# Kernel optimization log

Measured on AMD Instinct MI355X. Metric: run time of the kernel, lower is better.

## Reference

```python
import jax, jax.numpy as jnp
import numpy as np

EMBED_DIM = 1024
BATCH = 4
SEQ = 2048


def setup_inputs() -> dict:
    key = jax.random.key(0)
    ks = jax.random.split(key, 9)
    D = EMBED_DIM
    s = 1.0 / np.sqrt(D)
    inputs = jax.random.normal(ks[0], (BATCH, SEQ, D), dtype=jnp.float32)
    rotation_params = jax.random.normal(ks[1], (D, D), dtype=jnp.float32) * s
    entangle_params = jax.random.normal(ks[2], (D, D), dtype=jnp.float32) * s
    Wq = jax.random.normal(ks[3], (D, D), dtype=jnp.float32) * s
    bq = jax.random.normal(ks[4], (D,), dtype=jnp.float32) * 0.01
    Wk = jax.random.normal(ks[5], (D, D), dtype=jnp.float32) * s
    bk = jax.random.normal(ks[6], (D,), dtype=jnp.float32) * 0.01
    Wv = jax.random.normal(ks[7], (D, D), dtype=jnp.float32) * s
    bv = jax.random.normal(ks[8], (D,), dtype=jnp.float32) * 0.01
    # causal mask: True = masked out (matches torch masked_fill semantics)
    mask = jnp.triu(jnp.ones((SEQ, SEQ), dtype=bool), k=1)
    return {"inputs": inputs, "rotation_params": rotation_params,
            "entangle_params": entangle_params, "Wq": Wq, "bq": bq,
            "Wk": Wk, "bk": bk, "Wv": Wv, "bv": bv, "mask": mask}


def reference(inputs, rotation_params, entangle_params, Wq, bq, Wk, bk, Wv, bv, mask):
    D = inputs.shape[-1]
    # q = Linear(x) @ R^T ; k = Linear(x) @ E^T ; v = Linear(x)
    q = (jnp.einsum('bsd,ed->bse', inputs, Wq) + bq) @ rotation_params.T
    k = (jnp.einsum('bsd,ed->bse', inputs, Wk) + bk) @ entangle_params.T
    v = jnp.einsum('bsd,ed->bse', inputs, Wv) + bv
    scores = jnp.einsum('bqd,bkd->bqk', q, k) / jnp.sqrt(jnp.float32(D))
    scores = jnp.where(mask, jnp.float32(-jnp.inf), scores)
    probs = jax.nn.softmax(scores, axis=-1)  # dropout=0.0 -> identity
    return jnp.einsum('bqk,bkd->bqd', probs, v)
```

## Files before the change

kernel.cpp:

```cpp
#include <hip/hip_runtime.h>
#include <hip/hip_bf16.h>
#include <stdint.h>

#define DD 1024
#define SS 2048
#define BB 4

typedef __bf16 bf16;
typedef __bf16 bf16x8 __attribute__((ext_vector_type(8)));
typedef __bf16 bf16x4 __attribute__((ext_vector_type(4)));
typedef float f32x4 __attribute__((ext_vector_type(4)));

__device__ __forceinline__ void gload_lds16(const bf16* g, bf16* l) {
  __builtin_amdgcn_global_load_lds(
      (const __attribute__((address_space(1))) void*)g,
      (__attribute__((address_space(3))) void*)l, 16, 0, 0);
}

__global__ void cvt_all(const float* __restrict__ x, const float* __restrict__ R,
                        const float* __restrict__ E, const float* __restrict__ Wv,
                        bf16* __restrict__ xb, bf16* __restrict__ Rb,
                        bf16* __restrict__ Eb, bf16* __restrict__ Wvb) {
  int bid = blockIdx.x;
  const float* src;
  bf16* dst;
  int base;
  if (bid < 8192) { src = x; dst = xb; base = bid; }
  else if (bid < 9216) { src = R; dst = Rb; base = bid - 8192; }
  else if (bid < 10240) { src = E; dst = Eb; base = bid - 9216; }
  else { src = Wv; dst = Wvb; base = bid - 10240; }
  int i = (base * 256 + threadIdx.x) * 4;
  float4 v = *(const float4*)(src + i);
  bf16x4 o;
  o.x = (bf16)v.x; o.y = (bf16)v.y; o.z = (bf16)v.z; o.w = (bf16)v.w;
  *(bf16x4*)(dst + i) = o;
}

__global__ void transpose_cvt(const float* __restrict__ Wq,
                              const float* __restrict__ Wk,
                              bf16* __restrict__ WqT, bf16* __restrict__ WkT) {
  const float* src = blockIdx.z ? Wk : Wq;
  bf16* dst = blockIdx.z ? WkT : WqT;
  __shared__ float tile[32][33];
  int x = blockIdx.x * 32 + threadIdx.x;
  int y0 = blockIdx.y * 32;
  for (int r = threadIdx.y; r < 32; r += 8)
    tile[r][threadIdx.x] = src[(y0 + r) * DD + x];
  __syncthreads();
  int dx = blockIdx.y * 32 + threadIdx.x;
  int dy0 = blockIdx.x * 32;
  for (int r = threadIdx.y; r < 32; r += 8)
    dst[(dy0 + r) * DD + dx] = (bf16)tile[threadIdx.x][r];
}

__global__ void bias_fold(const float* __restrict__ R, const float* __restrict__ bq,
                          const float* __restrict__ E, const float* __restrict__ bk,
                          const float* __restrict__ bv, float* __restrict__ bias) {
  int e = blockIdx.x;
  if (e >= 2048) { if (threadIdx.x == 0) bias[e] = bv[e - 2048]; return; }
  const float* M = (e < 1024) ? R : E;
  const float* bb = (e < 1024) ? bq : bk;
  int row = e & 1023;
  float s = 0.f;
  for (int f = threadIdx.x; f < DD; f += 256) s += M[row * DD + f] * bb[f];
  for (int o = 32; o >= 1; o >>= 1) s += __shfl_xor(s, o, 64);
  __shared__ float red[4];
  if ((threadIdx.x & 63) == 0) red[threadIdx.x >> 6] = s;
  __syncthreads();
  if (threadIdx.x == 0) bias[e] = red[0] + red[1] + red[2] + red[3];
}

template <int MODE>
__global__ __launch_bounds__(256, 4)
void gemm_bt(const bf16* __restrict__ Ag, long lda, long sAb,
             const bf16* __restrict__ Bg, long ldb, long sBb,
             void* __restrict__ Cg, long ldc, long sCb,
             const float* __restrict__ bias, float scale, int K,
             bf16* __restrict__ vTp) {
  __shared__ __align__(16) bf16 smem[16384];
  bf16* As = smem;
  bf16* Bs = smem + 8192;

  int bx = blockIdx.x, by = blockIdx.y, bz = blockIdx.z;
  if (MODE == 1 && bx > by) return;
  long m0 = (long)by * 128, n0 = (long)bx * 128;
  const bf16* A = Ag + (long)bz * sAb + m0 * lda;
  const bf16* Bp = Bg + (long)bz * sBb + n0 * ldb;

  int t = threadIdx.x;
  int w = t >> 6, l = t & 63;
  int lr = l >> 2;
  int lc = (((l & 3) ^ (lr & 3)) * 8);
  int quad = l >> 4, ln = l & 15;
  int wm = w >> 1, wn = w & 1;
  int rdoff = ((quad ^ (ln & 3)) * 8);

  int Keff = (MODE == 2) ? (by + 1) * 128 : K;

  f32x4 acc[4][4];
#pragma unroll
  for (int i = 0; i < 4; i++)
#pragma unroll
    for (int j = 0; j < 4; j++) acc[i][j] = f32x4{0.f, 0.f, 0.f, 0.f};

  const bf16* a_base = As + (wm * 64 + ln) * 32 + rdoff;
  const bf16* b_base = Bs + (wn * 64 + ln) * 32 + rdoff;
  long arow0 = (long)(w * 16 + lr);

  for (int k0 = 0; k0 < Keff; k0 += 64) {
#pragma unroll
    for (int kk = 0; kk < 2; kk++) {
      int kc = k0 + kk * 32 + lc;
      gload_lds16(A + arow0 * lda + kc, As + kk * 4096 + w * 512);
      gload_lds16(A + (arow0 + 64) * lda + kc, As + kk * 4096 + 2048 + w * 512);
      gload_lds16(Bp + arow0 * ldb + kc, Bs + kk * 4096 + w * 512);
      gload_lds16(Bp + (arow0 + 64) * ldb + kc, Bs + kk * 4096 + 2048 + w * 512);
    }
    asm volatile("s_waitcnt vmcnt(0)" ::: "memory");
    __syncthreads();

#pragma unroll
    for (int kk = 0; kk < 2; kk++) {
      bf16x8 af[4], bfr[4];
#pragma unroll
      for (int i = 0; i < 4; i++) {
        af[i] = *(const bf16x8*)(a_base + kk * 4096 + i * 512);
        bfr[i] = *(const bf16x8*)(b_base + kk * 4096 + i * 512);
      }
#pragma unroll
      for (int i = 0; i < 4; i++)
#pragma unroll
        for (int j = 0; j < 4; j++)
          acc[i][j] = __builtin_amdgcn_mfma_f32_16x16x32_bf16(
              af[i], bfr[j], acc[i][j], 0, 0, 0);
    }
    __syncthreads();
  }

  if (MODE == 0) {
    if (vTp && n0 >= 2048) {
      int d0 = (int)n0 - 2048;
      int b = (int)(m0 >> 11);
      int s0 = (int)(m0 & 2047);
#pragma unroll
      for (int i = 0; i < 4; i++) {
        int sb = wm * 64 + i * 16 + quad * 4;
#pragma unroll
        for (int j = 0; j < 4; j++) {
          int d = wn * 64 + j * 16 + ln;
          float bv_ = bias[n0 + d];
#pragma unroll
          for (int r = 0; r < 4; r++)
            smem[d * 128 + ((sb + r) ^ (ln << 3))] = (bf16)(acc[i][j][r] + bv_);
        }
      }
      __syncthreads();
      int d = t >> 1, h = t & 1;
      bf16* dst = vTp + (long)b * DD * SS + (long)(d0 + d) * SS + s0 + h * 64;
#pragma unroll
      for (int j = 0; j < 8; j++) {
        int sbase = h * 64 + j * 8;
        bf16x8 v = *(const bf16x8*)(smem + d * 128 + (sbase ^ ((d & 15) << 3)));
        *(bf16x8*)(dst + j * 8) = v;
      }
    } else {
      bf16* C = (bf16*)Cg + (long)bz * sCb + m0 * ldc + n0;
#pragma unroll
      for (int i = 0; i < 4; i++) {
        int rb = wm * 64 + i * 16 + quad * 4;
#pragma unroll
        for (int j = 0; j < 4; j++) {
          int col = wn * 64 + j * 16 + ln;
          float bv_ = bias ? bias[n0 + col] : 0.f;
#pragma unroll
          for (int r = 0; r < 4; r++)
            C[(long)(rb + r) * ldc + col] = (bf16)(acc[i][j][r] + bv_);
        }
      }
    }
  } else {
    float* C = (float*)Cg + (long)bz * sCb + m0 * ldc + n0;
#pragma unroll
    for (int i = 0; i < 4; i++) {
      int rb = wm * 64 + i * 16 + quad * 4;
#pragma unroll
      for (int j = 0; j < 4; j++) {
        int col = wn * 64 + j * 16 + ln;
#pragma unroll
        for (int r = 0; r < 4; r++) {
          int row = rb + r;
          if (MODE == 1) {
            if (n0 + col <= m0 + row)
              C[(long)row * ldc + col] = acc[i][j][r] * scale;
          } else {
            C[(long)row * ldc + col] = acc[i][j][r];
          }
        }
      }
    }
  }
}

__global__ __launch_bounds__(256) void softmax_rows(float* __restrict__ scores) {
  long m = blockIdx.x;
  int i = (int)(m & (SS - 1));
  float* row = scores + m * SS;
  int t = threadIdx.x;
  int nvalid = i + 1;
  int base = t * 8;
  float x[8] = {0, 0, 0, 0, 0, 0, 0, 0};
  if (base < nvalid) {
    float4 v0 = *(const float4*)(row + base);
    float4 v1 = *(const float4*)(row + base + 4);
    x[0] = v0.x; x[1] = v0.y; x[2] = v0.z; x[3] = v0.w;
    x[4] = v1.x; x[5] = v1.y; x[6] = v1.z; x[7] = v1.w;
  }

  float mx = -INFINITY;
#pragma unroll
  for (int j = 0; j < 8; j++)
    if (base + j < nvalid) mx = fmaxf(mx, x[j]);
  for (int o = 32; o >= 1; o >>= 1) mx = fmaxf(mx, __shfl_xor(mx, o, 64));
  __shared__ float red[8];
  if ((t & 63) == 0) red[t >> 6] = mx;
  __syncthreads();
  mx = fmaxf(fmaxf(red[0], red[1]), fmaxf(red[2], red[3]));

  float e[8];
  float sum = 0.f;
#pragma unroll
  for (int j = 0; j < 8; j++) {
    e[j] = (base + j < nvalid) ? __expf(x[j] - mx) : 0.f;
    sum += e[j];
  }
  for (int o = 32; o >= 1; o >>= 1) sum += __shfl_xor(sum, o, 64);
  if ((t & 63) == 0) red[4 + (t >> 6)] = sum;
  __syncthreads();
  sum = red[4] + red[5] + red[6] + red[7];
  float inv = 1.f / sum;

  bf16x8 o8;
#pragma unroll
  for (int j = 0; j < 8; j++) o8[j] = (bf16)(e[j] * inv);
  *(bf16x8*)((bf16*)row + base) = o8;
}

extern "C" void kernel_launch(void* const* d_in, const int* in_sizes, int n_in,
                              void* d_out, int out_size, void* d_ws,
                              size_t ws_size, hipStream_t stream) {
  const float* x = (const float*)d_in[0];
  const float* R = (const float*)d_in[1];
  const float* E = (const float*)d_in[2];
  const float* Wq = (const float*)d_in[3];
  const float* bq = (const float*)d_in[4];
  const float* Wk = (const float*)d_in[5];
  const float* bk = (const float*)d_in[6];
  const float* Wv = (const float*)d_in[7];
  const float* bv = (const float*)d_in[8];
  float* out = (float*)d_out;

  char* ws = (char*)d_ws;
  bf16* qkv = (bf16*)ws;
  bf16* vT = (bf16*)(ws + 50331648);
  float* scores = (float*)(ws + 67108864);
  char* sr = ws + 67108864;
  bf16* xb = (bf16*)sr;
  bf16* Rb = (bf16*)(sr + 16777216);
  bf16* WqT = (bf16*)(sr + 20971520);
  bf16* wcat = (bf16*)(sr + 25165824);
  float* bias = (float*)(sr + 31457280);
  bf16* Eb = Rb + 1024 * 1024;
  bf16* WkT = WqT + 1024 * 1024;

  cvt_all<<<11264, 256, 0, stream>>>(x, R, E, Wv, xb, Rb, Eb, wcat + 2048 * DD);
  transpose_cvt<<<dim3(32, 32, 2), dim3(32, 8), 0, stream>>>(Wq, Wk, WqT, WkT);
  bias_fold<<<3072, 256, 0, stream>>>(R, bq, E, bk, bv, bias);

  gemm_bt<0><<<dim3(8, 8, 2), 256, 0, stream>>>(
      Rb, DD, 1024 * 1024, WqT, DD, 1024 * 1024, wcat, DD, 1024 * 1024,
      nullptr, 1.f, DD, nullptr);

  gemm_bt<0><<<dim3(24, 64, 1), 256, 0, stream>>>(xb, DD, 0, wcat, DD, 0, qkv,
                                                  3072, 0, bias, 1.f, DD, vT);

  gemm_bt<1><<<dim3(16, 16, BB), 256, 0, stream>>>(
      qkv, 3072, (long)SS * 3072, qkv + 1024, 3072, (long)SS * 3072, scores,
      SS, (long)SS * SS, nullptr, 0.03125f, DD, nullptr);

  softmax_rows<<<BB * SS, 256, 0, stream>>>(scores);

  gemm_bt<2><<<dim3(8, 16, BB), 256, 0, stream>>>(
      (const bf16*)scores, 4096, (long)SS * 4096, vT, SS, (long)DD * SS, out,
      DD, (long)SS * DD, nullptr, 1.f, SS, nullptr);
}
```

Measured before the change: 311.5 us.

## Add 256x128-tile GEMM with 32x32 MFMA for QKV and score products

Adds a new gemm_big kernel that uses 256x128 output tiles, a 64-wide K step, and 32x32x16 bf16 MFMA instructions. The QKV projection (including the transposed V write) and the causal QK^T score GEMM now use it. The larger tiles are meant to raise operand reuse and arithmetic intensity per LDS load, and the new MFMA shape issues fewer instructions. In exchange, occupancy drops (launch bounds 2), the grids have fewer blocks, and the causal skip works at coarser granularity, so more fully masked work may be computed.

```diff
diff --git a/kernel.cpp b/kernel.cpp
--- a/kernel.cpp
+++ b/kernel.cpp
@@ -10,6 +10,7 @@
 typedef __bf16 bf16x8 __attribute__((ext_vector_type(8)));
 typedef __bf16 bf16x4 __attribute__((ext_vector_type(4)));
 typedef float f32x4 __attribute__((ext_vector_type(4)));
+typedef float f32x16 __attribute__((ext_vector_type(16)));
 
 __device__ __forceinline__ void gload_lds16(const bf16* g, bf16* l) {
   __builtin_amdgcn_global_load_lds(
@@ -71,18 +72,145 @@
 }
 
 template <int MODE>
+__global__ __launch_bounds__(256, 2)
+void gemm_big(const bf16* __restrict__ Ag, long lda, long sAb,
+              const bf16* __restrict__ Bg, long ldb, long sBb,
+              void* __restrict__ Cg, long ldc, long sCb,
+              const float* __restrict__ bias, float scale, int K,
+              bf16* __restrict__ vTp) {
+  __shared__ __align__(16) bf16 As[256 * 64];
+  __shared__ __align__(16) bf16 Bs[128 * 64];
+
+  int bx = blockIdx.x, by = blockIdx.y, bz = blockIdx.z;
+  if (MODE == 1 && bx > 2 * by + 1) return;
+  long m0 = (long)by * 256, n0 = (long)bx * 128;
+  const bf16* A = Ag + (long)bz * sAb + m0 * lda;
+  const bf16* Bp = Bg + (long)bz * sBb + n0 * ldb;
+
+  int t = threadIdx.x;
+  int w = t >> 6, l = t & 63;
+  int lrow = l >> 3, lch = l & 7;
+  int swz = (lch ^ lrow) * 8;
+  int rl = l & 31, kh = l >> 5;
+  int wm = w >> 1, wn = w & 1;
+
+  f32x16 acc[4][2];
+#pragma unroll
+  for (int g = 0; g < 4; g++)
+#pragma unroll
+    for (int h = 0; h < 2; h++)
+#pragma unroll
+      for (int rr = 0; rr < 16; rr++) acc[g][h][rr] = 0.f;
+
+  for (int k0 = 0; k0 < K; k0 += 64) {
+#pragma unroll
+    for (int i = 0; i < 8; i++) {
+      int r0 = w * 64 + i * 8;
+      gload_lds16(A + (long)(r0 + lrow) * lda + k0 + swz, As + r0 * 64);
+    }
+#pragma unroll
+    for (int i = 0; i < 4; i++) {
+      int r0 = w * 32 + i * 8;
+      gload_lds16(Bp + (long)(r0 + lrow) * ldb + k0 + swz, Bs + r0 * 64);
+    }
+    asm volatile("s_waitcnt vmcnt(0)" ::: "memory");
+    __syncthreads();
+
+#pragma unroll
+    for (int kk = 0; kk < 4; kk++) {
+      int pos = ((kk * 2 + kh) ^ (rl & 7)) * 8;
+      bf16x8 af[4], bfr[2];
+#pragma unroll
+      for (int g = 0; g < 4; g++)
+        af[g] = *(const bf16x8*)(As + (wm * 128 + g * 32 + rl) * 64 + pos);
+#pragma unroll
+      for (int h = 0; h < 2; h++)
+        bfr[h] = *(const bf16x8*)(Bs + (wn * 64 + h * 32 + rl) * 64 + pos);
+#pragma unroll
+      for (int g = 0; g < 4; g++)
+#pragma unroll
+        for (int h = 0; h < 2; h++)
+          acc[g][h] = __builtin_amdgcn_mfma_f32_32x32x16_bf16(
+              af[g], bfr[h], acc[g][h], 0, 0, 0);
+    }
+    __syncthreads();
+  }
+
+  if (MODE == 0) {
+    if (vTp && n0 >= 2048) {
+      int d0 = (int)n0 - 2048;
+      int b = (int)(m0 >> 11);
+      int s0 = (int)(m0 & 2047);
+#pragma unroll
+      for (int hs = 0; hs < 2; hs++) {
+        if (wm == hs) {
+#pragma unroll
+          for (int g = 0; g < 4; g++)
+#pragma unroll
+            for (int h = 0; h < 2; h++) {
+              int d = wn * 64 + h * 32 + rl;
+              float bv_ = bias[n0 + d];
+#pragma unroll
+              for (int rr = 0; rr < 16; rr++) {
+                int s = g * 32 + (rr & 3) + 8 * (rr >> 2) + 4 * kh;
+                As[d * 128 + (s ^ ((d & 15) << 3))] = (bf16)(acc[g][h][rr] + bv_);
+              }
+            }
+        }
+        __syncthreads();
+        int d = t >> 1, hc = t & 1;
+        bf16* dst = vTp + (long)b * DD * SS + (long)(d0 + d) * SS + s0 + hs * 128;
+#pragma unroll
+        for (int j = 0; j < 8; j++) {
+          int sb = hc * 64 + j * 8;
+          bf16x8 v = *(const bf16x8*)(As + d * 128 + (sb ^ ((d & 15) << 3)));
+          *(bf16x8*)(dst + sb) = v;
+        }
+        __syncthreads();
+      }
+    } else {
+      bf16* C = (bf16*)Cg + (long)bz * sCb + m0 * ldc + n0;
+#pragma unroll
+      for (int g = 0; g < 4; g++)
+#pragma unroll
+        for (int h = 0; h < 2; h++) {
+          int col = wn * 64 + h * 32 + rl;
+          float bv_ = bias ? bias[n0 + col] : 0.f;
+#pragma unroll
+          for (int rr = 0; rr < 16; rr++) {
+            int row = wm * 128 + g * 32 + (rr & 3) + 8 * (rr >> 2) + 4 * kh;
+            C[(long)row * ldc + col] = (bf16)(acc[g][h][rr] + bv_);
+          }
+        }
+    }
+  } else {
+    float* C = (float*)Cg + (long)bz * sCb + m0 * ldc + n0;
+#pragma unroll
+    for (int g = 0; g < 4; g++)
+#pragma unroll
+      for (int h = 0; h < 2; h++) {
+        int col = wn * 64 + h * 32 + rl;
+#pragma unroll
+        for (int rr = 0; rr < 16; rr++) {
+          int row = wm * 128 + g * 32 + (rr & 3) + 8 * (rr >> 2) + 4 * kh;
+          if (n0 + col <= m0 + row)
+            C[(long)row * ldc + col] = acc[g][h][rr] * scale;
+        }
+      }
+  }
+}
+
+template <int MODE>
 __global__ __launch_bounds__(256, 4)
 void gemm_bt(const bf16* __restrict__ Ag, long lda, long sAb,
              const bf16* __restrict__ Bg, long ldb, long sBb,
              void* __restrict__ Cg, long ldc, long sCb,
-             const float* __restrict__ bias, float scale, int K,
-             bf16* __restrict__ vTp) {
+             const float* __restrict__ bias, float scale, int K) {
   __shared__ __align__(16) bf16 smem[16384];
   bf16* As = smem;
   bf16* Bs = smem + 8192;
 
   int bx = blockIdx.x, by = blockIdx.y, bz = blockIdx.z;
-  if (MODE == 1 && bx > by) return;
   long m0 = (long)by * 128, n0 = (long)bx * 128;
   const bf16* A = Ag + (long)bz * sAb + m0 * lda;
   const bf16* Bp = Bg + (long)bz * sBb + n0 * ldb;
@@ -138,44 +266,17 @@
   }
 
   if (MODE == 0) {
-    if (vTp && n0 >= 2048) {
-      int d0 = (int)n0 - 2048;
-      int b = (int)(m0 >> 11);
-      int s0 = (int)(m0 & 2047);
-#pragma unroll
-      for (int i = 0; i < 4; i++) {
-        int sb = wm * 64 + i * 16 + quad * 4;
-#pragma unroll
-        for (int j = 0; j < 4; j++) {
-          int d = wn * 64 + j * 16 + ln;
-          float bv_ = bias[n0 + d];
-#pragma unroll
-          for (int r = 0; r < 4; r++)
-            smem[d * 128 + ((sb + r) ^ (ln << 3))] = (bf16)(acc[i][j][r] + bv_);
-        }
-      }
-      __syncthreads();
-      int d = t >> 1, h = t & 1;
-      bf16* dst = vTp + (long)b * DD * SS + (long)(d0 + d) * SS + s0 + h * 64;
-#pragma unroll
-      for (int j = 0; j < 8; j++) {
-        int sbase = h * 64 + j * 8;
-        bf16x8 v = *(const bf16x8*)(smem + d * 128 + (sbase ^ ((d & 15) << 3)));
-        *(bf16x8*)(dst + j * 8) = v;
-      }
-    } else {
-      bf16* C = (bf16*)Cg + (long)bz * sCb + m0 * ldc + n0;
-#pragma unroll
-      for (int i = 0; i < 4; i++) {
-        int rb = wm * 64 + i * 16 + quad * 4;
-#pragma unroll
-        for (int j = 0; j < 4; j++) {
-          int col = wn * 64 + j * 16 + ln;
-          float bv_ = bias ? bias[n0 + col] : 0.f;
-#pragma unroll
-          for (int r = 0; r < 4; r++)
-            C[(long)(rb + r) * ldc + col] = (bf16)(acc[i][j][r] + bv_);
-        }
+    bf16* C = (bf16*)Cg + (long)bz * sCb + m0 * ldc + n0;
+#pragma unroll
+    for (int i = 0; i < 4; i++) {
+      int rb = wm * 64 + i * 16 + quad * 4;
+#pragma unroll
+      for (int j = 0; j < 4; j++) {
+        int col = wn * 64 + j * 16 + ln;
+        float bv_ = bias ? bias[n0 + col] : 0.f;
+#pragma unroll
+        for (int r = 0; r < 4; r++)
+          C[(long)(rb + r) * ldc + col] = (bf16)(acc[i][j][r] + bv_);
       }
     }
   } else {
@@ -187,15 +288,8 @@
       for (int j = 0; j < 4; j++) {
         int col = wn * 64 + j * 16 + ln;
 #pragma unroll
-        for (int r = 0; r < 4; r++) {
-          int row = rb + r;
-          if (MODE == 1) {
-            if (n0 + col <= m0 + row)
-              C[(long)row * ldc + col] = acc[i][j][r] * scale;
-          } else {
-            C[(long)row * ldc + col] = acc[i][j][r];
-          }
-        }
+        for (int r = 0; r < 4; r++)
+          C[(long)(rb + r) * ldc + col] = acc[i][j][r];
       }
     }
   }
@@ -278,12 +372,12 @@
 
   gemm_bt<0><<<dim3(8, 8, 2), 256, 0, stream>>>(
       Rb, DD, 1024 * 1024, WqT, DD, 1024 * 1024, wcat, DD, 1024 * 1024,
-      nullptr, 1.f, DD, nullptr);
-
-  gemm_bt<0><<<dim3(24, 64, 1), 256, 0, stream>>>(xb, DD, 0, wcat, DD, 0, qkv,
-                                                  3072, 0, bias, 1.f, DD, vT);
-
-  gemm_bt<1><<<dim3(16, 16, BB), 256, 0, stream>>>(
+      nullptr, 1.f, DD);
+
+  gemm_big<0><<<dim3(24, 32, 1), 256, 0, stream>>>(xb, DD, 0, wcat, DD, 0, qkv,
+                                                   3072, 0, bias, 1.f, DD, vT);
+
+  gemm_big<1><<<dim3(16, 8, BB), 256, 0, stream>>>(
       qkv, 3072, (long)SS * 3072, qkv + 1024, 3072, (long)SS * 3072, scores,
       SS, (long)SS * SS, nullptr, 0.03125f, DD, nullptr);
 
@@ -291,5 +385,5 @@
 
   gemm_bt<2><<<dim3(8, 16, BB), 256, 0, stream>>>(
       (const bf16*)scores, 4096, (long)SS * 4096, vT, SS, (long)DD * SS, out,
-      DD, (long)SS * DD, nullptr, 1.f, SS, nullptr);
-}
+      DD, (long)SS * DD, nullptr, 1.f, SS);
+}
```

After: 314.3 us. About the same (+0.9%).
